# Kernel tuning notes

Measured on AMD Instinct MI355X. Metric: run time of the kernel, lower is better.

The kernel has to match this reference:

```python
import jax, jax.numpy as jnp
import numpy as np

B, L = 16, 128
E, A = 34, 36          # num_events, num_arguments
V, D, H = 30000, 300, 256


def setup_inputs() -> dict:
    key = jax.random.key(0)
    ks = jax.random.split(key, 14)
    s = 0.08
    n = lambda k, shape: jax.random.normal(k, shape, jnp.float32) * s
    return {
        "input_ids": jax.random.randint(ks[0], (B, L), 0, V),
        "emb": n(ks[1], (V, D)),
        "Wih_f": n(ks[2], (4 * H, D)), "Whh_f": n(ks[3], (4 * H, H)),
        "bih_f": n(ks[4], (4 * H,)), "bhh_f": n(ks[5], (4 * H,)),
        "Wih_b": n(ks[6], (4 * H, D)), "Whh_b": n(ks[7], (4 * H, H)),
        "bih_b": n(ks[8], (4 * H,)), "bhh_b": n(ks[9], (4 * H,)),
        "We": n(ks[10], (E, 2 * H + E - 1)), "be": n(ks[11], (E,)),
        "Wa": n(ks[12], (A, 4 * H + A - 1 + E - 1)), "ba": n(ks[13], (A,)),
    }


def _lstm(x, Wih, Whh, bih, bhh):
    # x: [L, B, D] -> outputs [L, B, H]; PyTorch gate order i, f, g, o
    Bsz = x.shape[1]
    Hh = Whh.shape[1]
    b = bih + bhh

    def step(carry, xt):
        h, c = carry
        z = xt @ Wih.T + h @ Whh.T + b
        i, f, g, o = jnp.split(z, 4, axis=-1)
        c = jax.nn.sigmoid(f) * c + jax.nn.sigmoid(i) * jnp.tanh(g)
        h = jax.nn.sigmoid(o) * jnp.tanh(c)
        return (h, c), h

    h0 = jnp.zeros((Bsz, Hh), x.dtype)
    _, hs = jax.lax.scan(step, (h0, h0), x)
    return hs


def _forward(input_ids, emb, Wih_f, Whh_f, bih_f, bhh_f, Wih_b, Whh_b, bih_b, bhh_b, We, be, Wa, ba):
    Bsz, Ll = input_ids.shape
    x = emb[input_ids]                       # [B, L, D]
    xt = jnp.transpose(x, (1, 0, 2))         # [L, B, D]
    hf = _lstm(xt, Wih_f, Whh_f, bih_f, bhh_f)
    hb = _lstm(xt[::-1], Wih_b, Whh_b, bih_b, bhh_b)[::-1]
    hs = jnp.concatenate([hf, hb], axis=-1)  # [L, B, 2H]
    hidden = jnp.transpose(hs, (1, 0, 2))    # [B, L, 2H]

    ev_ids = jnp.arange(E - 1)
    ar_ids = jnp.arange(A - 1)
    g_trg0 = jnp.zeros((Bsz, E - 1), jnp.int32)
    g_trg_arg0 = jnp.zeros((Bsz, Ll, E - 1), jnp.int32)
    g_arg0 = jnp.zeros((Bsz, Ll, A - 1), jnp.int32)

    def step(carry, ht):                     # ht: [B, 2H] at position i
        g_trg, g_trg_arg, g_arg = carry
        ev_in = jnp.concatenate([ht, g_trg.astype(ht.dtype)], axis=1)
        ev_logit = ev_in @ We.T + be                       # [B, E]
        ev_pred = jnp.argmax(ev_logit, axis=-1)            # [B]
        trig = jnp.broadcast_to(ht[:, None, :], (Bsz, Ll, ht.shape[-1]))
        arg_in = jnp.concatenate(
            [hidden, trig, g_arg.astype(ht.dtype), g_trg_arg.astype(ht.dtype)], axis=2)
        arg_logits = arg_in @ Wa.T + ba                    # [B, L, A]
        arg_pred = jnp.argmax(arg_logits, axis=-1)         # [B, L]

        has_ev = ev_pred > 0
        # update_g_trg: g_trg[b, ev_pred[b]-1] = 1 where ev_pred>0
        g_trg = jnp.where(has_ev[:, None] & (ev_ids[None, :] == (ev_pred - 1)[:, None]), 1, g_trg)
        # update_g_trg_arg: column ev_pred-1 set to 1 where arg_pred>0
        cond_ta = (has_ev[:, None, None] & (arg_pred > 0)[:, :, None]
                   & (ev_ids[None, None, :] == (ev_pred - 1)[:, None, None]))
        g_trg_arg = jnp.where(cond_ta, 1, g_trg_arg)
        # update_g_arg: g_arg[b, j, arg_pred[b,j]-1] = 1 where ev_pred>0 and arg_pred>0
        cond_a = (has_ev[:, None, None] & (arg_pred > 0)[:, :, None]
                  & (ar_ids[None, None, :] == (arg_pred - 1)[:, :, None]))
        g_arg = jnp.where(cond_a, 1, g_arg)
        return (g_trg, g_trg_arg, g_arg), (ev_logit, arg_logits)

    _, (ev_all, arg_all) = jax.lax.scan(step, (g_trg0, g_trg_arg0, g_arg0), hs)
    event_logits = jnp.transpose(ev_all, (1, 0, 2))        # [B, L, E]
    arguments_logits = jnp.transpose(arg_all, (1, 0, 2, 3))  # [B, L, L, A]
    return event_logits, arguments_logits


def reference(input_ids, emb, Wih_f, Whh_f, bih_f, bhh_f, Wih_b, Whh_b, bih_b, bhh_b, We, be, Wa, ba):
    return _forward(input_ids, emb, Wih_f, Whh_f, bih_f, bhh_f,
                    Wih_b, Whh_b, bih_b, bhh_b, We, be, Wa, ba)
```

## Files before the change

kernel.cpp:

```cpp
#include <hip/hip_runtime.h>
#include <math.h>

#define B_  16
#define L_  128
#define E_  34
#define A_  36
#define D_  300
#define H_  256
#define KP_ 320
#define G4_ 1024
#define KC_ 512
#define NCAT_ 128
#define WAS_ 1092
#define WES_ 545

#define O_XH     0u
#define O_XL     327680u
#define O_WH_F   655360u
#define O_WH_B   819200u
#define O_WL_F   983040u
#define O_WL_B   1146880u
#define O_HX     1310720u
#define O_BSUM_F 1343488u
#define O_BSUM_B 1344512u
#define O_ZPRE   1345536u
#define O_HIDDEN 5539840u
#define O_WCAT   6588416u
#define O_BVEC   6653952u
#define O_P      6654080u
#define O_EVTAG  6916224u

#define HIX(k) ((k) + (((k) >> 5) << 2))

#define BARRIER_LGKM() asm volatile("s_waitcnt lgkmcnt(0)\n\ts_barrier" ::: "memory")

typedef short bf16x8 __attribute__((ext_vector_type(8)));
typedef float f32x4  __attribute__((ext_vector_type(4)));

__device__ __forceinline__ float fsig(float x) {
    return __builtin_amdgcn_rcpf(1.0f + __expf(-x));
}
__device__ __forceinline__ float ftanh(float x) {
    float e = __expf(-2.0f * fabsf(x));
    float t = (1.0f - e) * __builtin_amdgcn_rcpf(1.0f + e);
    return copysignf(t, x);
}
__device__ __forceinline__ unsigned short f2bf(float f) {
    unsigned u = __float_as_uint(f);
    return (unsigned short)((u + 0x7fffu + ((u >> 16) & 1u)) >> 16);
}
__device__ __forceinline__ float bf2f(unsigned short h) {
    return __uint_as_float(((unsigned)h) << 16);
}

__global__ void k_prep(const int* __restrict__ ids, const float* __restrict__ emb,
                       const float* __restrict__ Wih_f,
                       const float* __restrict__ bih_f, const float* __restrict__ bhh_f,
                       const float* __restrict__ Wih_b,
                       const float* __restrict__ bih_b, const float* __restrict__ bhh_b,
                       const float* __restrict__ We, const float* __restrict__ be,
                       const float* __restrict__ Wa, const float* __restrict__ ba,
                       float* __restrict__ ws) {
    const int N0 = 2048 * KP_;
    const int N1 = 2 * G4_ * KP_;
    const int N3 = 2 * 1024;
    const int N4 = 65536;
    const int N5 = 128;
    const int total = N0 + N1 + N3 + N4 + N5;
    unsigned short* xh = (unsigned short*)(ws + O_XH);
    unsigned short* xl = (unsigned short*)(ws + O_XL);
    for (int idx = blockIdx.x * blockDim.x + threadIdx.x; idx < total;
         idx += gridDim.x * blockDim.x) {
        int i = idx;
        if (i < N0) {
            int m = i / KP_, d = i - m * KP_;
            int t = m >> 4, b = m & 15;
            int id = ids[b * L_ + t];
            float f = (d < D_) ? emb[(size_t)id * D_ + d] : 0.0f;
            unsigned short h = f2bf(f);
            xh[i] = h;
            xl[i] = f2bf(f - bf2f(h));
            continue;
        }
        i -= N0;
        if (i < N1) {
            int dir = i / (G4_ * KP_), rem = i % (G4_ * KP_);
            int r = rem / KP_, k = rem - r * KP_;
            const float* Wih = dir ? Wih_b : Wih_f;
            unsigned short* wh = (unsigned short*)(ws + (dir ? O_WH_B : O_WH_F));
            unsigned short* wl = (unsigned short*)(ws + (dir ? O_WL_B : O_WL_F));
            float f = (k < D_) ? Wih[r * D_ + k] : 0.0f;
            unsigned short h = f2bf(f);
            wh[rem] = h;
            wl[rem] = f2bf(f - bf2f(h));
            continue;
        }
        i -= N1;
        if (i < N3) {
            int dir = i / 1024, r = i % 1024;
            ws[(dir ? O_BSUM_B : O_BSUM_F) + r] =
                (dir ? bih_b[r] + bhh_b[r] : bih_f[r] + bhh_f[r]);
            continue;
        }
        i -= N3;
        if (i < N4) {
            int k = i >> 7, n = i & 127;
            float v = 0.0f;
            if (n < 36)               v = Wa[n * WAS_ + k];
            else if (n < 72)          v = Wa[(n - 36) * WAS_ + KC_ + k];
            else if (n < 106)         v = We[(n - 72) * WES_ + k];
            ws[O_WCAT + i] = v;
            continue;
        }
        i -= N4;
        {
            float v = 0.0f;
            if (i < 36)               v = ba[i];
            else if (i >= 72 && i < 106) v = be[i - 72];
            ws[O_BVEC + i] = v;
        }
    }
}

__global__ __launch_bounds__(256) void k_gemm1(float* __restrict__ ws) {
    __shared__ unsigned short Ah[128][40];
    __shared__ unsigned short Al[128][40];
    __shared__ unsigned short Bh[128][40];
    __shared__ unsigned short Bl[128][40];
    int dir = blockIdx.z;
    int m0 = blockIdx.y * 128;
    int n0 = blockIdx.x * 128;
    int tid = threadIdx.x;
    const unsigned short* xh = (const unsigned short*)(ws + O_XH);
    const unsigned short* xl = (const unsigned short*)(ws + O_XL);
    const unsigned short* wh = (const unsigned short*)(ws + (dir ? O_WH_B : O_WH_F));
    const unsigned short* wl = (const unsigned short*)(ws + (dir ? O_WL_B : O_WL_F));
    const float* bsv = ws + (dir ? O_BSUM_B : O_BSUM_F);

    int w = tid >> 6, lane = tid & 63;
    int wr = w >> 1, wc = w & 1;
    int lr = lane & 15, lk = lane >> 4;

    int sr = tid >> 1, sh = tid & 1;
    int gm = m0 + sr;
    int tt = gm >> 4, bb2 = gm & 15;
    int srow = dir ? (((L_ - 1 - tt) << 4) | bb2) : gm;
    size_t aoff = (size_t)srow * KP_ + sh * 16;
    size_t boff = (size_t)(n0 + sr) * KP_ + sh * 16;
    int swb = sr * 80 + sh * 32;

    f32x4 acc[4][4] = {};
    for (int k0 = 0; k0 < KP_; k0 += 32) {
        float4 vah0 = *(const float4*)(xh + aoff + k0);
        float4 vah1 = *(const float4*)(xh + aoff + k0 + 8);
        float4 val0 = *(const float4*)(xl + aoff + k0);
        float4 val1 = *(const float4*)(xl + aoff + k0 + 8);
        float4 vbh0 = *(const float4*)(wh + boff + k0);
        float4 vbh1 = *(const float4*)(wh + boff + k0 + 8);
        float4 vbl0 = *(const float4*)(wl + boff + k0);
        float4 vbl1 = *(const float4*)(wl + boff + k0 + 8);
        *(float4*)((char*)&Ah[0][0] + swb) = vah0;
        *(float4*)((char*)&Ah[0][0] + swb + 16) = vah1;
        *(float4*)((char*)&Al[0][0] + swb) = val0;
        *(float4*)((char*)&Al[0][0] + swb + 16) = val1;
        *(float4*)((char*)&Bh[0][0] + swb) = vbh0;
        *(float4*)((char*)&Bh[0][0] + swb + 16) = vbh1;
        *(float4*)((char*)&Bl[0][0] + swb) = vbl0;
        *(float4*)((char*)&Bl[0][0] + swb + 16) = vbl1;
        __syncthreads();
        bf16x8 afh[4], afl[4], bfh[4], bfl[4];
#pragma unroll
        for (int mi = 0; mi < 4; mi++) {
            int rb = (wr * 64 + mi * 16 + lr) * 80 + lk * 16;
            afh[mi] = *(const bf16x8*)((const char*)&Ah[0][0] + rb);
            afl[mi] = *(const bf16x8*)((const char*)&Al[0][0] + rb);
        }
#pragma unroll
        for (int ni = 0; ni < 4; ni++) {
            int rb = (wc * 64 + ni * 16 + lr) * 80 + lk * 16;
            bfh[ni] = *(const bf16x8*)((const char*)&Bh[0][0] + rb);
            bfl[ni] = *(const bf16x8*)((const char*)&Bl[0][0] + rb);
        }
#pragma unroll
        for (int mi = 0; mi < 4; mi++)
#pragma unroll
            for (int ni = 0; ni < 4; ni++) {
                acc[mi][ni] = __builtin_amdgcn_mfma_f32_16x16x32_bf16(
                    afh[mi], bfh[ni], acc[mi][ni], 0, 0, 0);
                acc[mi][ni] = __builtin_amdgcn_mfma_f32_16x16x32_bf16(
                    afh[mi], bfl[ni], acc[mi][ni], 0, 0, 0);
                acc[mi][ni] = __builtin_amdgcn_mfma_f32_16x16x32_bf16(
                    afl[mi], bfh[ni], acc[mi][ni], 0, 0, 0);
            }
        __syncthreads();
    }
    float* zp = ws + O_ZPRE + (size_t)dir * 2048 * G4_;
    int crow = (lane >> 4) * 4;
#pragma unroll
    for (int ni = 0; ni < 4; ni++) {
        int n = n0 + wc * 64 + ni * 16 + lr;
        float bias = bsv[n];
#pragma unroll
        for (int mi = 0; mi < 4; mi++) {
            int mb = m0 + wr * 64 + mi * 16 + crow;
#pragma unroll
            for (int j = 0; j < 4; j++)
                zp[(size_t)(mb + j) * G4_ + n] = acc[mi][ni][j] + bias;
        }
    }
}

__global__ __launch_bounds__(512, 2) void k_lstm(float* __restrict__ ws,
                                                 const float* __restrict__ Whh_f,
                                                 const float* __restrict__ Whh_b) {
    int phys = blockIdx.x;
    int g    = phys >> 5;
    int cb   = phys & 31;
    int b    = cb & 15;
    int dir  = cb >> 4;
    int tid  = threadIdx.x;
    int rg   = tid >> 3;
    int kc   = tid & 7;

    const float* Whh  = dir ? Whh_b : Whh_f;
    const float* zpre = ws + O_ZPRE + (size_t)dir * 2048 * G4_;
    float* hid = ws + O_HIDDEN;
    unsigned long long* hx64 = (unsigned long long*)(ws + O_HX);

    __shared__ float h_sh[HIX(255) + 1 + 4];
    __shared__ float zbuf[256];

    int lr0  = rg << 2;
    int ggr0 = (lr0 >> 6) * 256 + g * 64 + (lr0 & 63);
    float4 w[4][8];
#pragma unroll
    for (int i = 0; i < 4; i++) {
        const float* wr = Whh + (size_t)(ggr0 + i) * H_ + (kc << 5);
#pragma unroll
        for (int c = 0; c < 8; c++) w[i][c] = *(const float4*)(wr + (c << 2));
    }
    for (int k = tid; k < HIX(255) + 1 + 4; k += 512) h_sh[k] = 0.0f;
    float c_state = 0.0f;
    float4 zv = make_float4(0.f, 0.f, 0.f, 0.f);
    if (kc == 0) zv = *(const float4*)(zpre + (size_t)(0 * B_ + b) * G4_ + ggr0);
    __syncthreads();

    for (int s = 0; s < L_; s++) {
        float4 zn = make_float4(0.f, 0.f, 0.f, 0.f);
        if (kc == 0 && s + 1 < L_)
            zn = *(const float4*)(zpre + (size_t)((s + 1) * B_ + b) * G4_ + ggr0);
        float a0 = 0.f, a1 = 0.f, a2 = 0.f, a3 = 0.f;
        const float* hp = &h_sh[kc * 36];
#pragma unroll
        for (int c = 0; c < 8; c++) {
            float4 hv = *(const float4*)(hp + (c << 2));
            a0 = fmaf(w[0][c].x, hv.x, a0); a0 = fmaf(w[0][c].y, hv.y, a0);
            a0 = fmaf(w[0][c].z, hv.z, a0); a0 = fmaf(w[0][c].w, hv.w, a0);
            a1 = fmaf(w[1][c].x, hv.x, a1); a1 = fmaf(w[1][c].y, hv.y, a1);
            a1 = fmaf(w[1][c].z, hv.z, a1); a1 = fmaf(w[1][c].w, hv.w, a1);
            a2 = fmaf(w[2][c].x, hv.x, a2); a2 = fmaf(w[2][c].y, hv.y, a2);
            a2 = fmaf(w[2][c].z, hv.z, a2); a2 = fmaf(w[2][c].w, hv.w, a2);
            a3 = fmaf(w[3][c].x, hv.x, a3); a3 = fmaf(w[3][c].y, hv.y, a3);
            a3 = fmaf(w[3][c].z, hv.z, a3); a3 = fmaf(w[3][c].w, hv.w, a3);
        }
#pragma unroll
        for (int m = 1; m < 8; m <<= 1) {
            a0 += __shfl_xor(a0, m); a1 += __shfl_xor(a1, m);
            a2 += __shfl_xor(a2, m); a3 += __shfl_xor(a3, m);
        }
        if (kc == 0) {
            float4 z4;
            z4.x = a0 + zv.x; z4.y = a1 + zv.y; z4.z = a2 + zv.z; z4.w = a3 + zv.w;
            *(float4*)&zbuf[lr0] = z4;
        }
        zv = zn;
        BARRIER_LGKM();
        int par = (s + 1) & 1;
        if (tid < 64) {
            float fi = fsig(zbuf[tid]);
            float ff = fsig(zbuf[tid + 64]);
            float gg = ftanh(zbuf[tid + 128]);
            float fo = fsig(zbuf[tid + 192]);
            c_state = ff * c_state + fi * gg;
            float h = fo * ftanh(c_state);
            int hr = g * 64 + tid;
            if (s + 1 < L_) {
                unsigned long long pk =
                    ((unsigned long long)(unsigned)(s + 1) << 32) | (unsigned)__float_as_uint(h);
                __hip_atomic_store(&hx64[(par << 13) + (phys << 6) + tid], pk,
                                   __ATOMIC_RELAXED, __HIP_MEMORY_SCOPE_AGENT);
            }
            h_sh[HIX(hr)] = h;
            int t_orig = dir ? (L_ - 1 - s) : s;
            hid[(size_t)(t_orig * B_ + b) * KC_ + dir * H_ + hr] = h;
        }
        if (tid >= 64 && tid < 256 && s + 1 < L_) {
            int which = tid >> 6;
            int sg = (g + which) & 3;
            int sb = cb | (sg << 5);
            int u  = tid & 63;
            const unsigned long long* wp = &hx64[(par << 13) + (sb << 6) + u];
            unsigned long long v;
            int cnt = 0;
            __builtin_amdgcn_s_sleep(6);
            do {
                v = __hip_atomic_load(wp, __ATOMIC_RELAXED, __HIP_MEMORY_SCOPE_AGENT);
            } while ((int)(v >> 32) < s + 1 && ++cnt < (1 << 20));
            h_sh[HIX(sg * 64 + u)] = __uint_as_float((unsigned)v);
        }
        BARRIER_LGKM();
    }
}

__global__ __launch_bounds__(256) void k_gemm2(float* __restrict__ ws) {
    __shared__ float As[16][64];
    __shared__ float Bs[16][64];
    int m0 = blockIdx.y * 64;
    int n0 = blockIdx.x * 64;
    int tid = threadIdx.x;
    const float* Ap = ws + O_HIDDEN;
    const float* Bp = ws + O_WCAT;
    const float* bv = ws + O_BVEC;
    float acc[4][4] = {};
    int a_m = tid >> 2, a_k = (tid & 3) << 2;
    int b_k = tid >> 4, b_n = (tid & 15) << 2;
    int ty = tid >> 4, tx = tid & 15;
    const float* arow = Ap + (size_t)(m0 + a_m) * KC_;
    for (int k0 = 0; k0 < KC_; k0 += 16) {
        float4 av = *(const float4*)(arow + k0 + a_k);
        float4 bvv = *(const float4*)(Bp + (size_t)(k0 + b_k) * NCAT_ + n0 + b_n);
        As[a_k + 0][a_m] = av.x; As[a_k + 1][a_m] = av.y;
        As[a_k + 2][a_m] = av.z; As[a_k + 3][a_m] = av.w;
        *(float4*)&Bs[b_k][b_n] = bvv;
        __syncthreads();
#pragma unroll
        for (int kk = 0; kk < 16; kk++) {
            float4 a4 = *(const float4*)&As[kk][ty * 4];
            float4 b4 = *(const float4*)&Bs[kk][tx * 4];
            acc[0][0] = fmaf(a4.x, b4.x, acc[0][0]); acc[0][1] = fmaf(a4.x, b4.y, acc[0][1]);
            acc[0][2] = fmaf(a4.x, b4.z, acc[0][2]); acc[0][3] = fmaf(a4.x, b4.w, acc[0][3]);
            acc[1][0] = fmaf(a4.y, b4.x, acc[1][0]); acc[1][1] = fmaf(a4.y, b4.y, acc[1][1]);
            acc[1][2] = fmaf(a4.y, b4.z, acc[1][2]); acc[1][3] = fmaf(a4.y, b4.w, acc[1][3]);
            acc[2][0] = fmaf(a4.z, b4.x, acc[2][0]); acc[2][1] = fmaf(a4.z, b4.y, acc[2][1]);
            acc[2][2] = fmaf(a4.z, b4.z, acc[2][2]); acc[2][3] = fmaf(a4.z, b4.w, acc[2][3]);
            acc[3][0] = fmaf(a4.w, b4.x, acc[3][0]); acc[3][1] = fmaf(a4.w, b4.y, acc[3][1]);
            acc[3][2] = fmaf(a4.w, b4.z, acc[3][2]); acc[3][3] = fmaf(a4.w, b4.w, acc[3][3]);
        }
        __syncthreads();
    }
    float4 bias = *(const float4*)(bv + n0 + tx * 4);
    float* Pp = ws + O_P + (size_t)m0 * NCAT_;
#pragma unroll
    for (int i = 0; i < 4; i++) {
        float4 o;
        o.x = acc[i][0] + bias.x; o.y = acc[i][1] + bias.y;
        o.z = acc[i][2] + bias.z; o.w = acc[i][3] + bias.w;
        *(float4*)(Pp + (size_t)(ty * 4 + i) * NCAT_ + n0 + tx * 4) = o;
    }
}

__global__ __launch_bounds__(1024) void k_dec(const float* __restrict__ We,
                                              const float* __restrict__ Wa,
                                              float* __restrict__ ws, float* __restrict__ out) {
    const float* P = ws + O_P;
    int* evtag = (int*)(ws + O_EVTAG);
    int lane = threadIdx.x & 63;
    if (blockIdx.x == 0) {
        int b = threadIdx.x >> 6;
        float Cg = 0.0f;
        unsigned long long gmask = 0ull;
        float pv = (lane < E_) ? P[(size_t)(0 * B_ + b) * NCAT_ + 72 + lane] : 0.0f;
        float p1 = (lane < E_) ? P[(size_t)(1 * B_ + b) * NCAT_ + 72 + lane] : 0.0f;
        for (int i = 0; i < L_; i++) {
            float p2 = 0.0f;
            if (i + 2 < L_ && lane < E_) p2 = P[(size_t)((i + 2) * B_ + b) * NCAT_ + 72 + lane];
            float v = (lane < E_) ? (pv + Cg) : -INFINITY;
            float mv = v;
            int mi = (lane < E_) ? lane : 0x7fffffff;
#pragma unroll
            for (int off = 32; off; off >>= 1) {
                float ov = __shfl_down(mv, off);
                int oi = __shfl_down(mi, off);
                if (ov > mv || (ov == mv && oi < mi)) { mv = ov; mi = oi; }
            }
            int p = __shfl(mi, 0);
            if (lane == 0)
                __hip_atomic_store(&evtag[b * L_ + i], ((i + 1) << 8) | p,
                                   __ATOMIC_RELAXED, __HIP_MEMORY_SCOPE_AGENT);
            if (lane < E_) out[(size_t)(b * L_ + i) * E_ + lane] = v;
            if (p > 0) {
                unsigned long long bit = 1ull << (p - 1);
                if (!(gmask & bit)) {
                    gmask |= bit;
                    if (lane < E_) Cg += We[lane * WES_ + 2 * H_ + (p - 1)];
                }
            }
            pv = p1; p1 = p2;
        }
    } else {
        int w = ((blockIdx.x - 1) << 4) + (threadIdx.x >> 6);
        int b = w >> 7, j = w & 127;
        float* outa = out + (size_t)B_ * L_ * E_;
        float C = 0.0f;
        if (lane < A_) C = P[(size_t)(j * B_ + b) * NCAT_ + lane];
        unsigned long long ga = 0ull, gta = 0ull;
        float tv = (lane < A_) ? P[(size_t)(0 * B_ + b) * NCAT_ + 36 + lane] : 0.0f;
        float t1 = (lane < A_) ? P[(size_t)(1 * B_ + b) * NCAT_ + 36 + lane] : 0.0f;
        int myv = (int)0x80000000;
        for (int i = 0; i < L_; i++) {
            float t2 = 0.0f;
            if (i + 2 < L_ && lane < A_) t2 = P[(size_t)((i + 2) * B_ + b) * NCAT_ + 36 + lane];
            int w0 = i & ~63;
            if ((i & 63) == 0)
                myv = __hip_atomic_load(&evtag[b * L_ + w0 + lane],
                                        __ATOMIC_RELAXED, __HIP_MEMORY_SCOPE_AGENT);
            int tv_tag = __shfl(myv, i & 63);
            if ((tv_tag >> 8) < i + 1) {
                int cnt = 0;
                do {
                    __builtin_amdgcn_s_sleep(1);
                    myv = __hip_atomic_load(&evtag[b * L_ + w0 + lane],
                                            __ATOMIC_RELAXED, __HIP_MEMORY_SCOPE_AGENT);
                    tv_tag = __shfl(myv, i & 63);
                } while ((tv_tag >> 8) < i + 1 && ++cnt < (1 << 18));
            }
            int ev = tv_tag & 0xff;
            float v = (lane < A_) ? (C + tv) : -INFINITY;
            float mv = v;
            int mi = (lane < A_) ? lane : 0x7fffffff;
#pragma unroll
            for (int off = 32; off; off >>= 1) {
                float ov = __shfl_down(mv, off);
                int oi = __shfl_down(mi, off);
                if (ov > mv || (ov == mv && oi < mi)) { mv = ov; mi = oi; }
            }
            int p = __shfl(mi, 0);
            if (lane < A_) outa[(size_t)((b * L_ + i) * L_ + j) * A_ + lane] = v;
            if (ev > 0 && p > 0) {
                unsigned long long bq = 1ull << (ev - 1);
                if (!(gta & bq)) {
                    gta |= bq;
                    if (lane < A_) C += Wa[lane * WAS_ + 4 * H_ + A_ - 1 + (ev - 1)];
                }
                unsigned long long br = 1ull << (p - 1);
                if (!(ga & br)) {
                    ga |= br;
                    if (lane < A_) C += Wa[lane * WAS_ + 4 * H_ + (p - 1)];
                }
            }
            tv = t1; t1 = t2;
        }
    }
}

extern "C" void kernel_launch(void* const* d_in, const int* in_sizes, int n_in,
                              void* d_out, int out_size, void* d_ws, size_t ws_size,
                              hipStream_t stream) {
    (void)in_sizes; (void)n_in; (void)out_size; (void)ws_size;
    const int*   ids   = (const int*)d_in[0];
    const float* emb   = (const float*)d_in[1];
    const float* Wih_f = (const float*)d_in[2];
    const float* Whh_f = (const float*)d_in[3];
    const float* bih_f = (const float*)d_in[4];
    const float* bhh_f = (const float*)d_in[5];
    const float* Wih_b = (const float*)d_in[6];
    const float* Whh_b = (const float*)d_in[7];
    const float* bih_b = (const float*)d_in[8];
    const float* bhh_b = (const float*)d_in[9];
    const float* We    = (const float*)d_in[10];
    const float* be    = (const float*)d_in[11];
    const float* Wa    = (const float*)d_in[12];
    const float* ba    = (const float*)d_in[13];
    float* out = (float*)d_out;
    float* ws  = (float*)d_ws;

    hipLaunchKernelGGL(k_prep, dim3(2048), dim3(256), 0, stream,
                       ids, emb, Wih_f, bih_f, bhh_f, Wih_b, bih_b, bhh_b,
                       We, be, Wa, ba, ws);
    hipLaunchKernelGGL(k_gemm1, dim3(8, 16, 2), dim3(256), 0, stream, ws);
    hipLaunchKernelGGL(k_lstm, dim3(128), dim3(512), 0, stream, ws, Whh_f, Whh_b);
    hipLaunchKernelGGL(k_gemm2, dim3(2, 32, 1), dim3(256), 0, stream, ws);
    hipLaunchKernelGGL(k_dec, dim3(129), dim3(1024), 0, stream, We, Wa, ws, out);
}
```

Before: 502.4 us.

## Fuse input-projection GEMM with LSTM recurrence using per-tile ready flags

The separate input GEMM and LSTM kernels are merged into one launch. Blocks 0-127 run the recurrence while the remaining 256 blocks compute the input-projection tiles, converting embeddings and weights to split bf16 on the fly instead of in a prep pass. Each GEMM tile publishes a counter in workspace that the recurrence blocks spin on before reading the next timestep's preactivations, so the recurrence can start before the whole GEMM finishes. This removes the large prep conversion pass and a kernel boundary, but it depends on all 384 blocks being co-resident and it adds atomic polling on the recurrence's critical path.

```diff
diff --git a/kernel.cpp b/kernel.cpp
--- a/kernel.cpp
+++ b/kernel.cpp
@@ -14,12 +14,6 @@
 #define WAS_ 1092
 #define WES_ 545
 
-#define O_XH     0u
-#define O_XL     327680u
-#define O_WH_F   655360u
-#define O_WH_B   819200u
-#define O_WL_F   983040u
-#define O_WL_B   1146880u
 #define O_HX     1310720u
 #define O_BSUM_F 1343488u
 #define O_BSUM_B 1344512u
@@ -29,6 +23,7 @@
 #define O_BVEC   6653952u
 #define O_P      6654080u
 #define O_EVTAG  6916224u
+#define O_ZTAG   6918272u
 
 #define HIX(k) ((k) + (((k) >> 5) << 2))
 
@@ -53,49 +48,19 @@
     return __uint_as_float(((unsigned)h) << 16);
 }
 
-__global__ void k_prep(const int* __restrict__ ids, const float* __restrict__ emb,
-                       const float* __restrict__ Wih_f,
-                       const float* __restrict__ bih_f, const float* __restrict__ bhh_f,
-                       const float* __restrict__ Wih_b,
+__global__ void k_prep(const float* __restrict__ bih_f, const float* __restrict__ bhh_f,
                        const float* __restrict__ bih_b, const float* __restrict__ bhh_b,
                        const float* __restrict__ We, const float* __restrict__ be,
                        const float* __restrict__ Wa, const float* __restrict__ ba,
                        float* __restrict__ ws) {
-    const int N0 = 2048 * KP_;
-    const int N1 = 2 * G4_ * KP_;
     const int N3 = 2 * 1024;
     const int N4 = 65536;
     const int N5 = 128;
-    const int total = N0 + N1 + N3 + N4 + N5;
-    unsigned short* xh = (unsigned short*)(ws + O_XH);
-    unsigned short* xl = (unsigned short*)(ws + O_XL);
+    const int N6 = 32;
+    const int total = N3 + N4 + N5 + N6;
     for (int idx = blockIdx.x * blockDim.x + threadIdx.x; idx < total;
          idx += gridDim.x * blockDim.x) {
         int i = idx;
-        if (i < N0) {
-            int m = i / KP_, d = i - m * KP_;
-            int t = m >> 4, b = m & 15;
-            int id = ids[b * L_ + t];
-            float f = (d < D_) ? emb[(size_t)id * D_ + d] : 0.0f;
-            unsigned short h = f2bf(f);
-            xh[i] = h;
-            xl[i] = f2bf(f - bf2f(h));
-            continue;
-        }
-        i -= N0;
-        if (i < N1) {
-            int dir = i / (G4_ * KP_), rem = i % (G4_ * KP_);
-            int r = rem / KP_, k = rem - r * KP_;
-            const float* Wih = dir ? Wih_b : Wih_f;
-            unsigned short* wh = (unsigned short*)(ws + (dir ? O_WH_B : O_WH_F));
-            unsigned short* wl = (unsigned short*)(ws + (dir ? O_WL_B : O_WL_F));
-            float f = (k < D_) ? Wih[r * D_ + k] : 0.0f;
-            unsigned short h = f2bf(f);
-            wh[rem] = h;
-            wl[rem] = f2bf(f - bf2f(h));
-            continue;
-        }
-        i -= N1;
         if (i < N3) {
             int dir = i / 1024, r = i % 1024;
             ws[(dir ? O_BSUM_B : O_BSUM_F) + r] =
@@ -113,202 +78,258 @@
             continue;
         }
         i -= N4;
-        {
+        if (i < N5) {
             float v = 0.0f;
             if (i < 36)               v = ba[i];
             else if (i >= 72 && i < 106) v = be[i - 72];
             ws[O_BVEC + i] = v;
-        }
+            continue;
+        }
+        i -= N5;
+        __hip_atomic_store(&((int*)(ws + O_ZTAG))[i], 0,
+                           __ATOMIC_RELAXED, __HIP_MEMORY_SCOPE_AGENT);
     }
 }
 
-__global__ __launch_bounds__(256) void k_gemm1(float* __restrict__ ws) {
-    __shared__ unsigned short Ah[128][40];
-    __shared__ unsigned short Al[128][40];
-    __shared__ unsigned short Bh[128][40];
-    __shared__ unsigned short Bl[128][40];
-    int dir = blockIdx.z;
-    int m0 = blockIdx.y * 128;
-    int n0 = blockIdx.x * 128;
+__global__ __launch_bounds__(512) void k_main(const int* __restrict__ ids,
+                                              const float* __restrict__ emb,
+                                              const float* __restrict__ Wih_f,
+                                              const float* __restrict__ Wih_b,
+                                              const float* __restrict__ Whh_f,
+                                              const float* __restrict__ Whh_b,
+                                              float* __restrict__ ws) {
+    __shared__ __align__(16) unsigned short smem[4 * 128 * 40];
+    int* ztag = (int*)(ws + O_ZTAG);
     int tid = threadIdx.x;
-    const unsigned short* xh = (const unsigned short*)(ws + O_XH);
-    const unsigned short* xl = (const unsigned short*)(ws + O_XL);
-    const unsigned short* wh = (const unsigned short*)(ws + (dir ? O_WH_B : O_WH_F));
-    const unsigned short* wl = (const unsigned short*)(ws + (dir ? O_WL_B : O_WL_F));
-    const float* bsv = ws + (dir ? O_BSUM_B : O_BSUM_F);
-
-    int w = tid >> 6, lane = tid & 63;
-    int wr = w >> 1, wc = w & 1;
-    int lr = lane & 15, lk = lane >> 4;
-
-    int sr = tid >> 1, sh = tid & 1;
-    int gm = m0 + sr;
-    int tt = gm >> 4, bb2 = gm & 15;
-    int srow = dir ? (((L_ - 1 - tt) << 4) | bb2) : gm;
-    size_t aoff = (size_t)srow * KP_ + sh * 16;
-    size_t boff = (size_t)(n0 + sr) * KP_ + sh * 16;
-    int swb = sr * 80 + sh * 32;
-
-    f32x4 acc[4][4] = {};
-    for (int k0 = 0; k0 < KP_; k0 += 32) {
-        float4 vah0 = *(const float4*)(xh + aoff + k0);
-        float4 vah1 = *(const float4*)(xh + aoff + k0 + 8);
-        float4 val0 = *(const float4*)(xl + aoff + k0);
-        float4 val1 = *(const float4*)(xl + aoff + k0 + 8);
-        float4 vbh0 = *(const float4*)(wh + boff + k0);
-        float4 vbh1 = *(const float4*)(wh + boff + k0 + 8);
-        float4 vbl0 = *(const float4*)(wl + boff + k0);
-        float4 vbl1 = *(const float4*)(wl + boff + k0 + 8);
-        *(float4*)((char*)&Ah[0][0] + swb) = vah0;
-        *(float4*)((char*)&Ah[0][0] + swb + 16) = vah1;
-        *(float4*)((char*)&Al[0][0] + swb) = val0;
-        *(float4*)((char*)&Al[0][0] + swb + 16) = val1;
-        *(float4*)((char*)&Bh[0][0] + swb) = vbh0;
-        *(float4*)((char*)&Bh[0][0] + swb + 16) = vbh1;
-        *(float4*)((char*)&Bl[0][0] + swb) = vbl0;
-        *(float4*)((char*)&Bl[0][0] + swb + 16) = vbl1;
+
+    if (blockIdx.x < 128) {
+        int phys = blockIdx.x;
+        int g    = phys >> 5;
+        int cb   = phys & 31;
+        int b    = cb & 15;
+        int dir  = cb >> 4;
+        int rg   = tid >> 3;
+        int kc   = tid & 7;
+
+        const float* Whh  = dir ? Whh_b : Whh_f;
+        const float* zpre = ws + O_ZPRE + (size_t)dir * 2048 * G4_;
+        float* hid = ws + O_HIDDEN;
+        unsigned long long* hx64 = (unsigned long long*)(ws + O_HX);
+
+        float* h_sh = (float*)smem;
+        float* zbuf = (float*)smem + 288;
+
+        int lr0  = rg << 2;
+        int ggr0 = (lr0 >> 6) * 256 + g * 64 + (lr0 & 63);
+        float4 w[4][8];
+#pragma unroll
+        for (int i = 0; i < 4; i++) {
+            const float* wr = Whh + (size_t)(ggr0 + i) * H_ + (kc << 5);
+#pragma unroll
+            for (int c = 0; c < 8; c++) w[i][c] = *(const float4*)(wr + (c << 2));
+        }
+        for (int k = tid; k < 288; k += 512) h_sh[k] = 0.0f;
+        float c_state = 0.0f;
+        int cur_tile = -1;
+        float4 zv = make_float4(0.f, 0.f, 0.f, 0.f);
+        if (kc == 0) {
+            int v, cnt = 0;
+            do {
+                v = __hip_atomic_load(&ztag[dir * 16], __ATOMIC_RELAXED,
+                                      __HIP_MEMORY_SCOPE_AGENT);
+                if (v < 8) __builtin_amdgcn_s_sleep(2);
+            } while (v < 8 && ++cnt < (1 << 22));
+            cur_tile = 0;
+            const unsigned long long* zr =
+                (const unsigned long long*)(zpre + (size_t)(0 * B_ + b) * G4_ + ggr0);
+            unsigned long long z0 = __hip_atomic_load(zr, __ATOMIC_RELAXED,
+                                                      __HIP_MEMORY_SCOPE_AGENT);
+            unsigned long long z1 = __hip_atomic_load(zr + 1, __ATOMIC_RELAXED,
+                                                      __HIP_MEMORY_SCOPE_AGENT);
+            zv.x = __uint_as_float((unsigned)z0); zv.y = __uint_as_float((unsigned)(z0 >> 32));
+            zv.z = __uint_as_float((unsigned)z1); zv.w = __uint_as_float((unsigned)(z1 >> 32));
+        }
         __syncthreads();
-        bf16x8 afh[4], afl[4], bfh[4], bfl[4];
-#pragma unroll
-        for (int mi = 0; mi < 4; mi++) {
-            int rb = (wr * 64 + mi * 16 + lr) * 80 + lk * 16;
-            afh[mi] = *(const bf16x8*)((const char*)&Ah[0][0] + rb);
-            afl[mi] = *(const bf16x8*)((const char*)&Al[0][0] + rb);
-        }
-#pragma unroll
-        for (int ni = 0; ni < 4; ni++) {
-            int rb = (wc * 64 + ni * 16 + lr) * 80 + lk * 16;
-            bfh[ni] = *(const bf16x8*)((const char*)&Bh[0][0] + rb);
-            bfl[ni] = *(const bf16x8*)((const char*)&Bl[0][0] + rb);
-        }
-#pragma unroll
-        for (int mi = 0; mi < 4; mi++)
-#pragma unroll
-            for (int ni = 0; ni < 4; ni++) {
-                acc[mi][ni] = __builtin_amdgcn_mfma_f32_16x16x32_bf16(
-                    afh[mi], bfh[ni], acc[mi][ni], 0, 0, 0);
-                acc[mi][ni] = __builtin_amdgcn_mfma_f32_16x16x32_bf16(
-                    afh[mi], bfl[ni], acc[mi][ni], 0, 0, 0);
-                acc[mi][ni] = __builtin_amdgcn_mfma_f32_16x16x32_bf16(
-                    afl[mi], bfh[ni], acc[mi][ni], 0, 0, 0);
-            }
+
+        for (int s = 0; s < L_; s++) {
+            float4 zn = make_float4(0.f, 0.f, 0.f, 0.f);
+            if (kc == 0 && s + 1 < L_) {
+                int nt = (s + 1) >> 3;
+                if (nt != cur_tile) {
+                    int v, cnt = 0;
+                    do {
+                        v = __hip_atomic_load(&ztag[dir * 16 + nt], __ATOMIC_RELAXED,
+                                              __HIP_MEMORY_SCOPE_AGENT);
+                        if (v < 8) __builtin_amdgcn_s_sleep(2);
+                    } while (v < 8 && ++cnt < (1 << 22));
+                    cur_tile = nt;
+                }
+                const unsigned long long* zr =
+                    (const unsigned long long*)(zpre + (size_t)((s + 1) * B_ + b) * G4_ + ggr0);
+                unsigned long long z0 = __hip_atomic_load(zr, __ATOMIC_RELAXED,
+                                                          __HIP_MEMORY_SCOPE_AGENT);
+                unsigned long long z1 = __hip_atomic_load(zr + 1, __ATOMIC_RELAXED,
+                                                          __HIP_MEMORY_SCOPE_AGENT);
+                zn.x = __uint_as_float((unsigned)z0); zn.y = __uint_as_float((unsigned)(z0 >> 32));
+                zn.z = __uint_as_float((unsigned)z1); zn.w = __uint_as_float((unsigned)(z1 >> 32));
+            }
+            float a0 = 0.f, a1 = 0.f, a2 = 0.f, a3 = 0.f;
+            const float* hp = &h_sh[kc * 36];
+#pragma unroll
+            for (int c = 0; c < 8; c++) {
+                float4 hv = *(const float4*)(hp + (c << 2));
+                a0 = fmaf(w[0][c].x, hv.x, a0); a0 = fmaf(w[0][c].y, hv.y, a0);
+                a0 = fmaf(w[0][c].z, hv.z, a0); a0 = fmaf(w[0][c].w, hv.w, a0);
+                a1 = fmaf(w[1][c].x, hv.x, a1); a1 = fmaf(w[1][c].y, hv.y, a1);
+                a1 = fmaf(w[1][c].z, hv.z, a1); a1 = fmaf(w[1][c].w, hv.w, a1);
+                a2 = fmaf(w[2][c].x, hv.x, a2); a2 = fmaf(w[2][c].y, hv.y, a2);
+                a2 = fmaf(w[2][c].z, hv.z, a2); a2 = fmaf(w[2][c].w, hv.w, a2);
+                a3 = fmaf(w[3][c].x, hv.x, a3); a3 = fmaf(w[3][c].y, hv.y, a3);
+                a3 = fmaf(w[3][c].z, hv.z, a3); a3 = fmaf(w[3][c].w, hv.w, a3);
+            }
+#pragma unroll
+            for (int m = 1; m < 8; m <<= 1) {
+                a0 += __shfl_xor(a0, m); a1 += __shfl_xor(a1, m);
+                a2 += __shfl_xor(a2, m); a3 += __shfl_xor(a3, m);
+            }
+            if (kc == 0) {
+                float4 z4;
+                z4.x = a0 + zv.x; z4.y = a1 + zv.y; z4.z = a2 + zv.z; z4.w = a3 + zv.w;
+                *(float4*)&zbuf[lr0] = z4;
+            }
+            zv = zn;
+            BARRIER_LGKM();
+            int par = (s + 1) & 1;
+            if (tid < 64) {
+                float fi = fsig(zbuf[tid]);
+                float ff = fsig(zbuf[tid + 64]);
+                float gg = ftanh(zbuf[tid + 128]);
+                float fo = fsig(zbuf[tid + 192]);
+                c_state = ff * c_state + fi * gg;
+                float h = fo * ftanh(c_state);
+                int hr = g * 64 + tid;
+                if (s + 1 < L_) {
+                    unsigned long long pk =
+                        ((unsigned long long)(unsigned)(s + 1) << 32) |
+                        (unsigned)__float_as_uint(h);
+                    __hip_atomic_store(&hx64[(par << 13) + (phys << 6) + tid], pk,
+                                       __ATOMIC_RELAXED, __HIP_MEMORY_SCOPE_AGENT);
+                }
+                h_sh[HIX(hr)] = h;
+                int t_orig = dir ? (L_ - 1 - s) : s;
+                hid[(size_t)(t_orig * B_ + b) * KC_ + dir * H_ + hr] = h;
+            }
+            if (tid >= 64 && tid < 256 && s + 1 < L_) {
+                int which = tid >> 6;
+                int sg = (g + which) & 3;
+                int sb = cb | (sg << 5);
+                int u  = tid & 63;
+                const unsigned long long* wp = &hx64[(par << 13) + (sb << 6) + u];
+                unsigned long long v;
+                int cnt = 0;
+                __builtin_amdgcn_s_sleep(6);
+                do {
+                    v = __hip_atomic_load(wp, __ATOMIC_RELAXED, __HIP_MEMORY_SCOPE_AGENT);
+                } while ((int)(v >> 32) < s + 1 && ++cnt < (1 << 20));
+                h_sh[HIX(sg * 64 + u)] = __uint_as_float((unsigned)v);
+            }
+            BARRIER_LGKM();
+        }
+    } else {
+        int gid = blockIdx.x - 128;
+        int dir = gid >> 7;
+        int rem = gid & 127;
+        int mtile = rem >> 3;
+        int m0 = mtile << 7;
+        int n0 = (rem & 7) << 7;
+        const float* Wih = dir ? Wih_b : Wih_f;
+        const float* bsv = ws + (dir ? O_BSUM_B : O_BSUM_F);
+
+        unsigned short* Ah = smem;
+        unsigned short* Al = smem + 5120;
+        unsigned short* Bh = smem + 10240;
+        unsigned short* Bl = smem + 15360;
+
+        int w = tid >> 6, lane = tid & 63;
+        int wr = w >> 2, wc = w & 3;
+        int lr = lane & 15, lk = lane >> 4;
+
+        int sr = tid >> 2, sh = tid & 3;
+        int gm = m0 + sr;
+        int tt = gm >> 4, bb2 = gm & 15;
+        int t_orig = dir ? (L_ - 1 - tt) : tt;
+        int aid = ids[bb2 * L_ + t_orig];
+        const float* arow = emb + (size_t)aid * D_;
+        const float* brow = Wih + (size_t)(n0 + sr) * D_;
+        int swb = sr * 80 + sh * 16;
+
+        f32x4 acc[4][2] = {};
+        for (int k0 = 0; k0 < KP_; k0 += 32) {
+            int cb0 = k0 + sh * 8;
+            bf16x8 vah, val, vbh, vbl;
+#pragma unroll
+            for (int e = 0; e < 8; e++) {
+                int c = cb0 + e;
+                float fa = (c < D_) ? arow[c] : 0.0f;
+                float fb = (c < D_) ? brow[c] : 0.0f;
+                unsigned short ha = f2bf(fa);
+                unsigned short hb = f2bf(fb);
+                vah[e] = (short)ha; val[e] = (short)f2bf(fa - bf2f(ha));
+                vbh[e] = (short)hb; vbl[e] = (short)f2bf(fb - bf2f(hb));
+            }
+            *(bf16x8*)((char*)Ah + swb) = vah;
+            *(bf16x8*)((char*)Al + swb) = val;
+            *(bf16x8*)((char*)Bh + swb) = vbh;
+            *(bf16x8*)((char*)Bl + swb) = vbl;
+            __syncthreads();
+            bf16x8 afh[4], afl[4], bfh[2], bfl[2];
+#pragma unroll
+            for (int mi = 0; mi < 4; mi++) {
+                int rb = (wr * 64 + mi * 16 + lr) * 80 + lk * 16;
+                afh[mi] = *(const bf16x8*)((const char*)Ah + rb);
+                afl[mi] = *(const bf16x8*)((const char*)Al + rb);
+            }
+#pragma unroll
+            for (int ni = 0; ni < 2; ni++) {
+                int rb = (wc * 32 + ni * 16 + lr) * 80 + lk * 16;
+                bfh[ni] = *(const bf16x8*)((const char*)Bh + rb);
+                bfl[ni] = *(const bf16x8*)((const char*)Bl + rb);
+            }
+#pragma unroll
+            for (int mi = 0; mi < 4; mi++)
+#pragma unroll
+                for (int ni = 0; ni < 2; ni++) {
+                    acc[mi][ni] = __builtin_amdgcn_mfma_f32_16x16x32_bf16(
+                        afh[mi], bfh[ni], acc[mi][ni], 0, 0, 0);
+                    acc[mi][ni] = __builtin_amdgcn_mfma_f32_16x16x32_bf16(
+                        afh[mi], bfl[ni], acc[mi][ni], 0, 0, 0);
+                    acc[mi][ni] = __builtin_amdgcn_mfma_f32_16x16x32_bf16(
+                        afl[mi], bfh[ni], acc[mi][ni], 0, 0, 0);
+                }
+            __syncthreads();
+        }
+        float* zp = ws + O_ZPRE + (size_t)dir * 2048 * G4_;
+        int crow = (lane >> 4) * 4;
+#pragma unroll
+        for (int ni = 0; ni < 2; ni++) {
+            int n = n0 + wc * 32 + ni * 16 + lr;
+            float bias = bsv[n];
+#pragma unroll
+            for (int mi = 0; mi < 4; mi++) {
+                int mb = m0 + wr * 64 + mi * 16 + crow;
+#pragma unroll
+                for (int j = 0; j < 4; j++) {
+                    float val2 = acc[mi][ni][j] + bias;
+                    __hip_atomic_store((unsigned*)(zp + (size_t)(mb + j) * G4_ + n),
+                                       __float_as_uint(val2),
+                                       __ATOMIC_RELAXED, __HIP_MEMORY_SCOPE_AGENT);
+                }
+            }
+        }
         __syncthreads();
-    }
-    float* zp = ws + O_ZPRE + (size_t)dir * 2048 * G4_;
-    int crow = (lane >> 4) * 4;
-#pragma unroll
-    for (int ni = 0; ni < 4; ni++) {
-        int n = n0 + wc * 64 + ni * 16 + lr;
-        float bias = bsv[n];
-#pragma unroll
-        for (int mi = 0; mi < 4; mi++) {
-            int mb = m0 + wr * 64 + mi * 16 + crow;
-#pragma unroll
-            for (int j = 0; j < 4; j++)
-                zp[(size_t)(mb + j) * G4_ + n] = acc[mi][ni][j] + bias;
-        }
-    }
-}
-
-__global__ __launch_bounds__(512, 2) void k_lstm(float* __restrict__ ws,
-                                                 const float* __restrict__ Whh_f,
-                                                 const float* __restrict__ Whh_b) {
-    int phys = blockIdx.x;
-    int g    = phys >> 5;
-    int cb   = phys & 31;
-    int b    = cb & 15;
-    int dir  = cb >> 4;
-    int tid  = threadIdx.x;
-    int rg   = tid >> 3;
-    int kc   = tid & 7;
-
-    const float* Whh  = dir ? Whh_b : Whh_f;
-    const float* zpre = ws + O_ZPRE + (size_t)dir * 2048 * G4_;
-    float* hid = ws + O_HIDDEN;
-    unsigned long long* hx64 = (unsigned long long*)(ws + O_HX);
-
-    __shared__ float h_sh[HIX(255) + 1 + 4];
-    __shared__ float zbuf[256];
-
-    int lr0  = rg << 2;
-    int ggr0 = (lr0 >> 6) * 256 + g * 64 + (lr0 & 63);
-    float4 w[4][8];
-#pragma unroll
-    for (int i = 0; i < 4; i++) {
-        const float* wr = Whh + (size_t)(ggr0 + i) * H_ + (kc << 5);
-#pragma unroll
-        for (int c = 0; c < 8; c++) w[i][c] = *(const float4*)(wr + (c << 2));
-    }
-    for (int k = tid; k < HIX(255) + 1 + 4; k += 512) h_sh[k] = 0.0f;
-    float c_state = 0.0f;
-    float4 zv = make_float4(0.f, 0.f, 0.f, 0.f);
-    if (kc == 0) zv = *(const float4*)(zpre + (size_t)(0 * B_ + b) * G4_ + ggr0);
-    __syncthreads();
-
-    for (int s = 0; s < L_; s++) {
-        float4 zn = make_float4(0.f, 0.f, 0.f, 0.f);
-        if (kc == 0 && s + 1 < L_)
-            zn = *(const float4*)(zpre + (size_t)((s + 1) * B_ + b) * G4_ + ggr0);
-        float a0 = 0.f, a1 = 0.f, a2 = 0.f, a3 = 0.f;
-        const float* hp = &h_sh[kc * 36];
-#pragma unroll
-        for (int c = 0; c < 8; c++) {
-            float4 hv = *(const float4*)(hp + (c << 2));
-            a0 = fmaf(w[0][c].x, hv.x, a0); a0 = fmaf(w[0][c].y, hv.y, a0);
-            a0 = fmaf(w[0][c].z, hv.z, a0); a0 = fmaf(w[0][c].w, hv.w, a0);
-            a1 = fmaf(w[1][c].x, hv.x, a1); a1 = fmaf(w[1][c].y, hv.y, a1);
-            a1 = fmaf(w[1][c].z, hv.z, a1); a1 = fmaf(w[1][c].w, hv.w, a1);
-            a2 = fmaf(w[2][c].x, hv.x, a2); a2 = fmaf(w[2][c].y, hv.y, a2);
-            a2 = fmaf(w[2][c].z, hv.z, a2); a2 = fmaf(w[2][c].w, hv.w, a2);
-            a3 = fmaf(w[3][c].x, hv.x, a3); a3 = fmaf(w[3][c].y, hv.y, a3);
-            a3 = fmaf(w[3][c].z, hv.z, a3); a3 = fmaf(w[3][c].w, hv.w, a3);
-        }
-#pragma unroll
-        for (int m = 1; m < 8; m <<= 1) {
-            a0 += __shfl_xor(a0, m); a1 += __shfl_xor(a1, m);
-            a2 += __shfl_xor(a2, m); a3 += __shfl_xor(a3, m);
-        }
-        if (kc == 0) {
-            float4 z4;
-            z4.x = a0 + zv.x; z4.y = a1 + zv.y; z4.z = a2 + zv.z; z4.w = a3 + zv.w;
-            *(float4*)&zbuf[lr0] = z4;
-        }
-        zv = zn;
-        BARRIER_LGKM();
-        int par = (s + 1) & 1;
-        if (tid < 64) {
-            float fi = fsig(zbuf[tid]);
-            float ff = fsig(zbuf[tid + 64]);
-            float gg = ftanh(zbuf[tid + 128]);
-            float fo = fsig(zbuf[tid + 192]);
-            c_state = ff * c_state + fi * gg;
-            float h = fo * ftanh(c_state);
-            int hr = g * 64 + tid;
-            if (s + 1 < L_) {
-                unsigned long long pk =
-                    ((unsigned long long)(unsigned)(s + 1) << 32) | (unsigned)__float_as_uint(h);
-                __hip_atomic_store(&hx64[(par << 13) + (phys << 6) + tid], pk,
-                                   __ATOMIC_RELAXED, __HIP_MEMORY_SCOPE_AGENT);
-            }
-            h_sh[HIX(hr)] = h;
-            int t_orig = dir ? (L_ - 1 - s) : s;
-            hid[(size_t)(t_orig * B_ + b) * KC_ + dir * H_ + hr] = h;
-        }
-        if (tid >= 64 && tid < 256 && s + 1 < L_) {
-            int which = tid >> 6;
-            int sg = (g + which) & 3;
-            int sb = cb | (sg << 5);
-            int u  = tid & 63;
-            const unsigned long long* wp = &hx64[(par << 13) + (sb << 6) + u];
-            unsigned long long v;
-            int cnt = 0;
-            __builtin_amdgcn_s_sleep(6);
-            do {
-                v = __hip_atomic_load(wp, __ATOMIC_RELAXED, __HIP_MEMORY_SCOPE_AGENT);
-            } while ((int)(v >> 32) < s + 1 && ++cnt < (1 << 20));
-            h_sh[HIX(sg * 64 + u)] = __uint_as_float((unsigned)v);
-        }
-        BARRIER_LGKM();
+        if (tid == 0)
+            __hip_atomic_fetch_add(&ztag[dir * 16 + mtile], 1,
+                                   __ATOMIC_RELEASE, __HIP_MEMORY_SCOPE_AGENT);
     }
 }
 
@@ -474,11 +495,10 @@
     float* out = (float*)d_out;
     float* ws  = (float*)d_ws;
 
-    hipLaunchKernelGGL(k_prep, dim3(2048), dim3(256), 0, stream,
-                       ids, emb, Wih_f, bih_f, bhh_f, Wih_b, bih_b, bhh_b,
-                       We, be, Wa, ba, ws);
-    hipLaunchKernelGGL(k_gemm1, dim3(8, 16, 2), dim3(256), 0, stream, ws);
-    hipLaunchKernelGGL(k_lstm, dim3(128), dim3(512), 0, stream, ws, Whh_f, Whh_b);
+    hipLaunchKernelGGL(k_prep, dim3(64), dim3(256), 0, stream,
+                       bih_f, bhh_f, bih_b, bhh_b, We, be, Wa, ba, ws);
+    hipLaunchKernelGGL(k_main, dim3(384), dim3(512), 0, stream,
+                       ids, emb, Wih_f, Wih_b, Whh_f, Whh_b, ws);
     hipLaunchKernelGGL(k_gemm2, dim3(2, 32, 1), dim3(256), 0, stream, ws);
     hipLaunchKernelGGL(k_dec, dim3(129), dim3(1024), 0, stream, We, Wa, ws, out);
 }
```

Result: slower. 575.8 us (+14.6%).
